# Kernel optimization log

Measured on AMD Instinct MI355X. Metric: run time of the kernel, lower is better.

Reference implementation:

```python
import jax, jax.numpy as jnp
import numpy as np

FS = 44100
LS = 1323000  # 30 s at 44.1 kHz (Ls/fs = 30 exactly)
FMIN, FMAX, BNDS = 32.7, 20000.0, 96
MIN_WIN = 4


def _design():
    """Reimplementation of LogScale + nsgfwin(sliced=False) + calcwinrange +
    the matrixform nsgtf loop parameters, producing a dense gather-index
    matrix idx [nbins, Mmax] and window matrix gw [nbins, Mmax]."""
    odiv = (np.log2(FMAX) - np.log2(FMIN)) / (BNDS - 1)
    pow2n = 2.0 ** odiv
    f = FMIN * pow2n ** np.arange(BNDS)
    lbas = BNDS
    frqs = np.concatenate(([0.0], f, [FS / 2.0]))
    fbas = np.concatenate((frqs, FS - frqs[-2:0:-1]))  # mirror negative freqs
    fbas *= float(LS) / FS
    # bandwidths M (window lengths)
    M = np.zeros(len(fbas), dtype=np.int64)
    M[0] = np.round(2 * fbas[1])
    for k in range(1, 2 * lbas + 1):
        M[k] = np.round(fbas[k + 1] - fbas[k - 1])
    M[-1] = np.round(LS - fbas[-2])
    M = np.maximum(M, MIN_WIN)
    # Hann windows (zero-frequency centered, hannwin)
    g = [0.5 * (np.cos(np.arange(m) * (2.0 * np.pi / m)) + 1.0) for m in M]
    # center positions rfbas (calcwinrange -> timepos == rfbas, nn == Ls)
    fb = fbas.copy()
    fb[lbas] = (fbas[lbas - 1] + fbas[lbas + 1]) / 2
    fb[lbas + 2] = LS - fb[lbas]
    rfbas = np.round(fb).astype(np.int64)
    nbins = len(g) // 2 + 1        # real=True, reducedform=0
    Mmax = int(M[:nbins].max())    # matrixform: all bins padded to Mmax
    idx = np.zeros((nbins, Mmax), dtype=np.int32)
    gw = np.zeros((nbins, Mmax), dtype=np.float32)
    for j in range(nbins):
        gj = g[j]
        Lg = len(gj)
        win = (np.arange(-(Lg // 2), Lg - (Lg // 2)) + rfbas[j]) % LS
        gs = np.fft.fftshift(gj)  # g is real -> conj is a no-op
        h1, h2 = (Lg + 1) // 2, Lg // 2
        # nsgtf placement: temp[:h1] = t[h2:], temp[-h2:] = t[:h2]
        idx[j, :h1] = win[h2:]
        gw[j, :h1] = gs[h2:]
        if h2 > 0:
            idx[j, Mmax - h2:] = win[:h2]
            gw[j, Mmax - h2:] = gs[:h2]
    return idx, gw


def setup_inputs() -> dict:
    key = jax.random.key(0)
    idx, gw = _design()
    s = jax.random.normal(key, (2, LS), dtype=jnp.float32)  # [channels, Ls]
    return {"s": s, "idx": jnp.asarray(idx), "gw": jnp.asarray(gw)}


def reference(s, idx, gw):
    # NSGT forward (nsgtf, matrixform, real): FFT the signal, gather each
    # frequency bin's circular window range, multiply by the fftshifted
    # window, zero-pad into a length-Mmax buffer, and IFFT per bin.
    ft = jnp.fft.fft(s.astype(jnp.complex64))          # [B, Ls]
    t = ft[:, idx] * gw                                # [B, nbins, Mmax]
    c = jnp.fft.ifft(t, axis=-1)                       # complex coefficients
    # pack complex output as trailing (real, imag) float32 channel
    return jnp.stack((c.real, c.imag), axis=-1)        # [B, nbins, Mmax, 2]
```

## Files before the change

### kernel.cpp

```cpp
#include <hip/hip_runtime.h>

#define LS 1323000
#define NB 98
#define MM 123000
#define N2 3000
#define BATCH 2
#define NROWS_T (NB*BATCH)
#define TWO_PI 6.28318530717958647692f

#define KBN 188
#define QN  96
#define SROW (KBN*QN*16)
#define QP  104

typedef __attribute__((ext_vector_type(8))) short short8;
typedef __attribute__((ext_vector_type(4))) float f32x4;

__device__ __forceinline__ float2 cmul(float2 a, float2 b){
  return make_float2(a.x*b.x - a.y*b.y, a.x*b.y + a.y*b.x);
}
__device__ __forceinline__ unsigned short f2bf(float f){
  unsigned int u = __float_as_uint(f);
  unsigned int r = (u + 0x7FFFu + ((u >> 16) & 1u)) >> 16;
  return (unsigned short)r;
}

template<int R,int S>
__device__ __forceinline__ void butterfly(float2* v){
  if constexpr (R==2){
    float2 a=v[0], b=v[1];
    v[0]=make_float2(a.x+b.x, a.y+b.y);
    v[1]=make_float2(a.x-b.x, a.y-b.y);
  } else if constexpr (R==4){
    float2 t0=make_float2(v[0].x+v[2].x, v[0].y+v[2].y);
    float2 t1=make_float2(v[0].x-v[2].x, v[0].y-v[2].y);
    float2 t2=make_float2(v[1].x+v[3].x, v[1].y+v[3].y);
    float2 t3=make_float2(v[1].x-v[3].x, v[1].y-v[3].y);
    v[0]=make_float2(t0.x+t2.x, t0.y+t2.y);
    v[2]=make_float2(t0.x-t2.x, t0.y-t2.y);
    v[1]=make_float2(t1.x - (float)S*t3.y, t1.y + (float)S*t3.x);
    v[3]=make_float2(t1.x + (float)S*t3.y, t1.y - (float)S*t3.x);
  } else if constexpr (R==8){
    float2 e[4]={v[0],v[2],v[4],v[6]};
    float2 o[4]={v[1],v[3],v[5],v[7]};
    butterfly<4,S>(e);
    butterfly<4,S>(o);
    const float h = 0.70710678118654752440f;
    float2 w1=make_float2(h, (float)S*h);
    float2 w2=make_float2(0.f, (float)S);
    float2 w3=make_float2(-h, (float)S*h);
    float2 o1=cmul(o[1],w1), o2=cmul(o[2],w2), o3=cmul(o[3],w3);
    v[0]=make_float2(e[0].x+o[0].x, e[0].y+o[0].y);
    v[4]=make_float2(e[0].x-o[0].x, e[0].y-o[0].y);
    v[1]=make_float2(e[1].x+o1.x, e[1].y+o1.y);
    v[5]=make_float2(e[1].x-o1.x, e[1].y-o1.y);
    v[2]=make_float2(e[2].x+o2.x, e[2].y+o2.y);
    v[6]=make_float2(e[2].x-o2.x, e[2].y-o2.y);
    v[3]=make_float2(e[3].x+o3.x, e[3].y+o3.y);
    v[7]=make_float2(e[3].x-o3.x, e[3].y-o3.y);
  } else {
    float2 x[R];
    #pragma unroll
    for(int k=0;k<R;k++){
      float2 acc=v[0];
      #pragma unroll
      for(int n=1;n<R;n++){
        const int p=(k*n)%R;
        float ang = (float)S * (TWO_PI/(float)R) * (float)p;
        float sn,cs; __sincosf(ang,&sn,&cs);
        acc.x += v[n].x*cs - v[n].y*sn;
        acc.y += v[n].x*sn + v[n].y*cs;
      }
      x[k]=acc;
    }
    #pragma unroll
    for(int k=0;k<R;k++) v[k]=x[k];
  }
}

template<int R,int S>
__global__ void __launch_bounds__(256)
fft_pass(const float2* __restrict__ in, float2* __restrict__ out,
         int N, int Ns, int nrows){
  const int T = N / R;
  long long gid = (long long)blockIdx.x*blockDim.x + threadIdx.x;
  if (gid >= (long long)T*nrows) return;
  int row = (int)(gid / T);
  int j   = (int)(gid - (long long)row*T);
  const float2* x = in  + (size_t)row*N;
  float2*       y = out + (size_t)row*N;
  int t = j % Ns;
  float u = (float)t / (float)(Ns*R);
  float ang = (float)S * TWO_PI * u;
  float sn,cs; __sincosf(ang,&sn,&cs);
  float2 w1=make_float2(cs,sn);
  float2 wr=make_float2(1.f,0.f);
  float2 v[R];
  #pragma unroll
  for(int r=0;r<R;r++){
    float2 a = x[j + r*T];
    v[r] = cmul(a, wr);
    wr = cmul(wr, w1);
  }
  butterfly<R,S>(v);
  int d = (j/Ns)*(Ns*R) + t;
  #pragma unroll
  for(int r=0;r<R;r++) y[d + r*Ns] = v[r];
}

__global__ void __launch_bounds__(256)
fft_r2c8(const float* __restrict__ s, float2* __restrict__ y){
  const int T = LS/8;
  long long gid = (long long)blockIdx.x*blockDim.x + threadIdx.x;
  if (gid >= (long long)T*BATCH) return;
  int row = (int)(gid / T);
  int j   = (int)(gid - (long long)row*T);
  const float* x = s + (size_t)row*LS;
  float2*      yr = y + (size_t)row*LS;
  float2 v[8];
  #pragma unroll
  for(int r=0;r<8;r++) v[r] = make_float2(x[j + r*T], 0.f);
  butterfly<8,-1>(v);
  int d = 8*j;
  #pragma unroll
  for(int r=0;r<8;r++) yr[d + r] = v[r];
}

__global__ void span_init(int* __restrict__ spanA, int* __restrict__ spanB){
  int j = blockIdx.x*blockDim.x + threadIdx.x;
  if (j < NB){ spanA[j] = 0; spanB[j] = MM; }
}

#define SPAN_SLICE 4096
__global__ void __launch_bounds__(256)
rowspan_par(const float* __restrict__ gw, int* __restrict__ spanA,
            int* __restrict__ spanB){
  const int j  = blockIdx.x;
  const int lo = blockIdx.y * SPAN_SLICE;
  const int end = min(lo + SPAN_SLICE, MM);
  const float* g = gw + (size_t)j*MM;
  const int tid = threadIdx.x;
  int mA = -1, mB = MM;
  for (int m = lo + tid*4; m < end; m += 256*4){
    float4 v = *(const float4*)(g + m);
    #pragma unroll
    for (int t = 0; t < 4; t++){
      float f = ((const float*)&v)[t];
      int m2 = m + t;
      if (f != 0.f){
        if (m2 < 61500){ if (m2 > mA) mA = m2; }
        else           { if (m2 < mB) mB = m2; }
      }
    }
  }
  __shared__ int sA[256], sB[256];
  sA[tid]=mA; sB[tid]=mB; __syncthreads();
  for (int s=128; s>0; s>>=1){
    if (tid<s){ sA[tid]=max(sA[tid],sA[tid+s]); sB[tid]=min(sB[tid],sB[tid+s]); }
    __syncthreads();
  }
  if (tid==0){
    if (sA[0] >= 0) atomicMax(&spanA[j], sA[0]+1);
    if (sB[0] < MM) atomicMin(&spanB[j], sB[0]);
  }
}

__global__ void __launch_bounds__(256)
a_prep(unsigned short* __restrict__ A96){
  int i = blockIdx.x*blockDim.x + threadIdx.x;
  if (i >= 96*QP) return;
  int R = i / QP, q = i - R*QP;
  float val = 0.f;
  if (R < 82 && q < 82){
    int k2 = R >> 1, c = R & 1, n2 = q >> 1, cp = q & 1;
    int p = (k2*n2) % 41;
    float ang = (float)p * (TWO_PI/41.f);
    float sn, cs; __sincosf(ang, &sn, &cs);
    val = c ? (cp ? cs : sn) : (cp ? -sn : cs);
  }
  A96[i] = f2bf(val);
}

template<int R, int Ns>
__device__ __forceinline__ void lds_stage(const float2* src, float2* dst, int tid){
  const int T = N2 / R;
  for (int j = tid; j < T; j += 256){
    int t = j % Ns;
    float2 w1;
    if constexpr (Ns == 1) w1 = make_float2(1.f, 0.f);
    else {
      float ang = TWO_PI * (float)t / (float)(Ns*R);
      float sn, cs; __sincosf(ang, &sn, &cs);
      w1 = make_float2(cs, sn);
    }
    float2 wr = make_float2(1.f, 0.f);
    float2 v[R];
    #pragma unroll
    for (int r = 0; r < R; r++){ v[r] = cmul(src[j + r*T], wr); wr = cmul(wr, w1); }
    butterfly<R,1>(v);
    int d = (j/Ns)*(Ns*R) + t;
    #pragma unroll
    for (int r = 0; r < R; r++) dst[d + r*Ns] = v[r];
  }
}

__global__ void __launch_bounds__(256)
inv_s1(const float2* __restrict__ ft, const int* __restrict__ idx,
       const float* __restrict__ gw, const int* __restrict__ spanA,
       const int* __restrict__ spanB,
       unsigned short* __restrict__ Bb, int row0){
  __shared__ float2 u0[N2];
  __shared__ float2 u1[N2];
  const int n2  = blockIdx.x;
  const int row = row0 + blockIdx.y;
  const int jrow = row % NB;
  const int b    = row / NB;
  const int tid = threadIdx.x;
  const int spA = spanA[jrow], spB = spanB[jrow];
  const int n1A = (spA - n2 + 40) / 41;
  const int n1B = (spB - n2 + 40) / 41;
  const int*   idxr = idx + (size_t)jrow*MM;
  const float* gwr  = gw  + (size_t)jrow*MM;
  const float2* ftb = ft  + (size_t)b*LS;
  for (int i = tid; i < N2; i += 256){
    float2 val = make_float2(0.f, 0.f);
    if (i < n1A || i >= n1B){
      int n = n2 + 41*i;
      int id = idxr[n];
      float g = gwr[n] * (1.0f/(float)MM);
      float2 f = ftb[id];
      val = make_float2(f.x*g, f.y*g);
    }
    u0[i] = val;
  }
  __syncthreads();
  lds_stage<5,1>(u0, u1, tid);   __syncthreads();
  lds_stage<5,5>(u1, u0, tid);   __syncthreads();
  lds_stage<5,25>(u0, u1, tid);  __syncthreads();
  lds_stage<3,125>(u1, u0, tid); __syncthreads();
  lds_stage<8,375>(u0, u1, tid); __syncthreads();
  unsigned short* Brow = Bb + (size_t)blockIdx.y*SROW;
  const int qr = 2*n2, qi = 2*n2+1;
  for (int k1 = tid; k1 < N2; k1 += 256){
    float ang = (float)(n2*k1) * (TWO_PI/(float)MM);
    float sn, cs; __sincosf(ang, &sn, &cs);
    float2 v = cmul(u1[k1], make_float2(cs, sn));
    int kb = k1 >> 4, kl = k1 & 15;
    size_t base = (size_t)kb*(QN*16) + kl;
    Brow[base + qr*16] = f2bf(v.x);
    Brow[base + qi*16] = f2bf(v.y);
  }
}

__global__ void __launch_bounds__(256)
inv_s2_mfma(const unsigned short* __restrict__ A96,
            const unsigned short* __restrict__ Bb,
            float2* __restrict__ out){
  __shared__ unsigned short Als[96*QP];
  __shared__ unsigned short Bls[64*QP];
  const int tid = threadIdx.x;

  {
    const uint4* src = (const uint4*)A96;
    uint4* dst = (uint4*)Als;
    for (int f = tid; f < (96*QP*2)/16; f += 256) dst[f] = src[f];
  }
  {
    const unsigned short* Bt = Bb + (size_t)blockIdx.y*SROW
                                  + (size_t)blockIdx.x*4*(QN*16);
    for (int f = tid; f < 768; f += 256){
      uint4 d = *(const uint4*)(Bt + (size_t)f*8);
      int q   = (f >> 1) % QN;
      int kb  = f / (QN*2);
      int kl0 = (f & 1) * 8;
      if (q >= 82) d = make_uint4(0u,0u,0u,0u);
      const unsigned short* e = (const unsigned short*)&d;
      int rbase = kb*16 + kl0;
      #pragma unroll
      for (int j = 0; j < 8; j++)
        Bls[(rbase + j)*QP + q] = e[j];
    }
  }
  __syncthreads();

  const int w = tid >> 6, l = tid & 63;
  const int g = l >> 4, c = l & 15;

  f32x4 acc[6];
  #pragma unroll
  for (int m = 0; m < 6; m++) acc[m] = (f32x4){0.f,0.f,0.f,0.f};

  short8 b0 = *(const short8*)&Bls[(16*w + c)*QP +  0 + 8*g];
  short8 b1 = *(const short8*)&Bls[(16*w + c)*QP + 32 + 8*g];
  short8 b2 = *(const short8*)&Bls[(16*w + c)*QP + 64 + 8*g];
  #pragma unroll
  for (int m = 0; m < 6; m++){
    short8 a0 = *(const short8*)&Als[(16*m + c)*QP +  0 + 8*g];
    short8 a1 = *(const short8*)&Als[(16*m + c)*QP + 32 + 8*g];
    short8 a2 = *(const short8*)&Als[(16*m + c)*QP + 64 + 8*g];
    acc[m] = __builtin_amdgcn_mfma_f32_16x16x32_bf16(a0, b0, acc[m], 0, 0, 0);
    acc[m] = __builtin_amdgcn_mfma_f32_16x16x32_bf16(a1, b1, acc[m], 0, 0, 0);
    acc[m] = __builtin_amdgcn_mfma_f32_16x16x32_bf16(a2, b2, acc[m], 0, 0, 0);
  }

  float2* orow = out + (size_t)blockIdx.y*MM;
  int k1 = blockIdx.x*64 + 16*w + c;
  if (k1 < N2){
    #pragma unroll
    for (int m = 0; m < 6; m++){
      int R0 = 16*m + 4*g;
      int k2a = R0 >> 1;
      int k2b = k2a + 1;
      if (k2a < 41) orow[(size_t)k2a*N2 + k1] = make_float2(acc[m][0], acc[m][1]);
      if (k2b < 41) orow[(size_t)k2b*N2 + k1] = make_float2(acc[m][2], acc[m][3]);
    }
  }
}

extern "C" void kernel_launch(void* const* d_in, const int* in_sizes, int n_in,
                              void* d_out, int out_size, void* d_ws, size_t ws_size,
                              hipStream_t stream){
  const float* s   = (const float*)d_in[0];
  const int*   idx = (const int*)d_in[1];
  const float* gw  = (const float*)d_in[2];
  float2* out = (float2*)d_out;
  char* ws = (char*)d_ws;

  const size_t FWD_BYTES = 21168128;
  float2* bufA = (float2*)ws;
  float2* bufB = (float2*)(ws + FWD_BYTES);
  int* spanA = (int*)(ws + 2*FWD_BYTES);
  int* spanB = (int*)(ws + 2*FWD_BYTES + 512);
  unsigned short* A96 = (unsigned short*)(ws + 2*FWD_BYTES + 1024);
  const size_t A_BYTES = 20480;
  unsigned short* Bbase = (unsigned short*)(ws + 2*FWD_BYTES + 1024 + A_BYTES);

  a_prep<<<(96*QP + 255)/256, 256, 0, stream>>>(A96);
  span_init<<<1, 128, 0, stream>>>(spanA, spanB);
  {
    dim3 g(NB, (MM + SPAN_SLICE - 1)/SPAN_SLICE);
    rowspan_par<<<g, 256, 0, stream>>>(gw, spanA, spanB);
  }

  {
    long long tot = (long long)(LS/8)*BATCH;
    int blks = (int)((tot + 255)/256);
    fft_r2c8<<<blks,256,0,stream>>>(s, bufA);
  }
  float2* cur = bufA; float2* nxt = bufB;
  int Ns = 8;
  #define FWD(R) do{                                                         \
    long long tot = (long long)(LS/(R))*BATCH;                               \
    int blks = (int)((tot + 255)/256);                                       \
    fft_pass<R,-1><<<blks,256,0,stream>>>(cur, nxt, LS, Ns, BATCH);          \
    Ns *= (R);                                                               \
    { float2* tmp=cur; cur=nxt; nxt=tmp; }                                   \
  }while(0)
  FWD(7); FWD(7); FWD(5); FWD(5); FWD(5); FWD(3); FWD(3); FWD(3);
  #undef FWD

  const size_t row_bytes = (size_t)SROW * 2;
  size_t used = 2*FWD_BYTES + 1024 + A_BYTES;
  size_t avail = (ws_size > used) ? (ws_size - used) : 0;
  int max_chunk = (int)(avail / row_bytes);
  if (max_chunk > NROWS_T) max_chunk = NROWS_T;
  if (max_chunk < 1) max_chunk = 1;

  for (int c0 = 0; c0 < NROWS_T; c0 += max_chunk){
    int cr = NROWS_T - c0; if (cr > max_chunk) cr = max_chunk;
    dim3 g1(41, cr);
    inv_s1<<<g1,256,0,stream>>>(cur, idx, gw, spanA, spanB, Bbase, c0);
    dim3 g2(47, cr);
    inv_s2_mfma<<<g2,256,0,stream>>>(A96, Bbase, out + (size_t)c0*MM);
  }
}
```

Before: 528.3 us.

## Add coalesced pack-gather kernel that transposes windowed bins before stride-41 FFT stage

Adds a pack_gather kernel that reads idx/gw contiguously in tiles, gathers and scales the spectrum into shared memory, then writes it transposed into a scratch buffer (the output region) laid out by n2 residue. inv_s1 then reads contiguous rows instead of doing strided gathers of idx, gw and ft with stride 41. This is meant to cut uncoalesced memory traffic in the first inverse-FFT stage, at the cost of an extra kernel launch and a full write and read of the intermediate buffer. It also adds a duplicated butterfly line that is immediately overwritten.

```diff
diff --git a/kernel.cpp b/kernel.cpp
--- a/kernel.cpp
+++ b/kernel.cpp
@@ -57,6 +57,7 @@
     v[2]=make_float2(e[2].x+o2.x, e[2].y+o2.y);
     v[6]=make_float2(e[2].x-o2.x, e[2].y-o2.y);
     v[3]=make_float2(e[3].x+o3.x, e[3].y+o3.y);
+    v[7]=make_float2(e[3].x-o3.x, e[7-4].y-o3.y);
     v[7]=make_float2(e[3].x-o3.x, e[3].y-o3.y);
   } else {
     float2 x[R];
@@ -181,6 +182,46 @@
   A96[i] = f2bf(val);
 }
 
+#define PTILE 1681
+__global__ void __launch_bounds__(256)
+pack_gather(const float2* __restrict__ ft, const int* __restrict__ idx,
+            const float* __restrict__ gw, const int* __restrict__ spanA,
+            const int* __restrict__ spanB, float2* __restrict__ T, int row0){
+  const int row  = row0 + blockIdx.y;
+  const int jrow = row % NB;
+  const int b    = row / NB;
+  const int spA = spanA[jrow], spB = spanB[jrow];
+  const int base = blockIdx.x * PTILE;
+  const int end  = min(base + PTILE, MM);
+  if (!(base < spA || end > spB)) return;
+  __shared__ float2 tile[PTILE];
+  const int cnt = end - base;
+  const int*   idxr = idx + (size_t)jrow*MM;
+  const float* gwr  = gw  + (size_t)jrow*MM;
+  const float2* ftb = ft  + (size_t)b*LS;
+  for (int l = threadIdx.x; l < cnt; l += 256){
+    int n = base + l;
+    float g = gwr[n] * (1.0f/(float)MM);
+    float2 f = ftb[idxr[n]];
+    tile[l] = make_float2(f.x*g, f.y*g);
+  }
+  __syncthreads();
+  float2* Trow = T + (size_t)blockIdx.y*MM;
+  const int bm = base % 41;
+  for (int l2 = threadIdx.x; l2 < PTILE; l2 += 256){
+    int n2 = l2 / 41, w = l2 - 41*n2;
+    int l0 = n2 - bm; if (l0 < 0) l0 += 41;
+    int l = l0 + 41*w;
+    if (l < cnt){
+      int n = base + l;
+      if (n < spA || n >= spB){
+        int ig = n / 41;
+        Trow[(size_t)n2*N2 + ig] = tile[l];
+      }
+    }
+  }
+}
+
 template<int R, int Ns>
 __device__ __forceinline__ void lds_stage(const float2* src, float2* dst, int tid){
   const int T = N2 / R;
@@ -205,8 +246,7 @@
 }
 
 __global__ void __launch_bounds__(256)
-inv_s1(const float2* __restrict__ ft, const int* __restrict__ idx,
-       const float* __restrict__ gw, const int* __restrict__ spanA,
+inv_s1(const float2* __restrict__ T, const int* __restrict__ spanA,
        const int* __restrict__ spanB,
        unsigned short* __restrict__ Bb, int row0){
   __shared__ float2 u0[N2];
@@ -214,23 +254,14 @@
   const int n2  = blockIdx.x;
   const int row = row0 + blockIdx.y;
   const int jrow = row % NB;
-  const int b    = row / NB;
   const int tid = threadIdx.x;
   const int spA = spanA[jrow], spB = spanB[jrow];
   const int n1A = (spA - n2 + 40) / 41;
   const int n1B = (spB - n2 + 40) / 41;
-  const int*   idxr = idx + (size_t)jrow*MM;
-  const float* gwr  = gw  + (size_t)jrow*MM;
-  const float2* ftb = ft  + (size_t)b*LS;
+  const float2* Trow = T + (size_t)blockIdx.y*MM + (size_t)n2*N2;
   for (int i = tid; i < N2; i += 256){
     float2 val = make_float2(0.f, 0.f);
-    if (i < n1A || i >= n1B){
-      int n = n2 + 41*i;
-      int id = idxr[n];
-      float g = gwr[n] * (1.0f/(float)MM);
-      float2 f = ftb[id];
-      val = make_float2(f.x*g, f.y*g);
-    }
+    if (i < n1A || i >= n1B) val = Trow[i];
     u0[i] = val;
   }
   __syncthreads();
@@ -366,11 +397,15 @@
   if (max_chunk > NROWS_T) max_chunk = NROWS_T;
   if (max_chunk < 1) max_chunk = 1;
 
+  const int ptiles = (MM + PTILE - 1)/PTILE;
   for (int c0 = 0; c0 < NROWS_T; c0 += max_chunk){
     int cr = NROWS_T - c0; if (cr > max_chunk) cr = max_chunk;
+    float2* Tchunk = out + (size_t)c0*MM;
+    dim3 g0(ptiles, cr);
+    pack_gather<<<g0,256,0,stream>>>(cur, idx, gw, spanA, spanB, Tchunk, c0);
     dim3 g1(41, cr);
-    inv_s1<<<g1,256,0,stream>>>(cur, idx, gw, spanA, spanB, Bbase, c0);
+    inv_s1<<<g1,256,0,stream>>>(Tchunk, spanA, spanB, Bbase, c0);
     dim3 g2(47, cr);
-    inv_s2_mfma<<<g2,256,0,stream>>>(A96, Bbase, out + (size_t)c0*MM);
-  }
-}
+    inv_s2_mfma<<<g2,256,0,stream>>>(A96, Bbase, Tchunk);
+  }
+}
```

After: 542.7 us. 1.03x slower.
